# Kernel tuning notes

Hardware: AMD Instinct MI355X
Metric: run time of the kernel (lower is better)

## Reference

```python
import jax, jax.numpy as jnp
import numpy as np


def setup_inputs() -> dict:
    key = jax.random.key(0)
    ks = jax.random.split(key, 5)
    B, H, W, C, R = 4, 64, 64, 256, 32
    x = jax.random.normal(ks[0], (B, H, W, C), dtype=jnp.float32)
    # 1x1 conv kernels stored as [C_in, C_out] matrices (equivalent math)
    w_f = jax.random.normal(ks[1], (C, R), dtype=jnp.float32) * (1.0 / np.sqrt(C))
    w_g = jax.random.normal(ks[2], (C, R), dtype=jnp.float32) * (1.0 / np.sqrt(C))
    w_h = jax.random.normal(ks[3], (C, R), dtype=jnp.float32) * (1.0 / np.sqrt(C))
    w_v = jax.random.normal(ks[4], (R, C), dtype=jnp.float32) * (1.0 / np.sqrt(R))
    gamma = jnp.zeros((1,), dtype=jnp.float32)
    return {"x": x, "w_f": w_f, "w_g": w_g, "w_h": w_h, "w_v": w_v, "gamma": gamma}


def reference(x, w_f, w_g, w_h, w_v, gamma):
    B, H, W, C = x.shape
    N = H * W
    xt = x.reshape(B, N, C)                       # flatten spatial tokens
    f = jnp.einsum('bnc,cr->bnr', xt, w_f)        # 1x1 conv == token-wise matmul
    g = jnp.einsum('bnc,cr->bnr', xt, w_g)
    h = jnp.einsum('bnc,cr->bnr', xt, w_h)
    scores = jnp.einsum('bnr,bmr->bnm', f, g)     # [B, N, N]
    # NOTE: original softmaxes over axis=1 (the query/row axis), not axis=-1
    attn = jax.nn.softmax(scores, axis=1)
    y = jnp.einsum('bnm,bmr->bnr', attn, h)       # [B, N, R]
    y = jnp.einsum('bnr,rc->bnc', y, w_v)         # output 1x1 conv
    y = y.reshape(B, H, W, C)
    return gamma * y + x
```

## Files before the change

kernel.cpp:

```cpp
#include <hip/hip_runtime.h>


#define BB 4
#define NN 4096
#define CC 256
#define RR 32
#define CSEG 4
#define MP 40
#define LOG2E 1.44269504088896340736f

typedef short short8 __attribute__((ext_vector_type(8)));
typedef unsigned short ushort8 __attribute__((ext_vector_type(8)));
typedef float floatx4 __attribute__((ext_vector_type(4)));

#define MFMA16 __builtin_amdgcn_mfma_f32_16x16x32_bf16

static __device__ __forceinline__ unsigned short f2bf(float f) {
  union { float f; unsigned u; } v; v.f = f;
  const unsigned r = v.u + 0x7fffu + ((v.u >> 16) & 1u);
  return (unsigned short)(r >> 16);
}
static __device__ __forceinline__ unsigned bfpack(float lo, float hi) {
  return __builtin_amdgcn_perm(__float_as_uint(hi), __float_as_uint(lo), 0x07060302u);
}

__global__ __launch_bounds__(256) void k_fgh(
    const float* __restrict__ x, const float* __restrict__ wf,
    const float* __restrict__ wg, const float* __restrict__ wh,
    const float* __restrict__ wv,
    unsigned short* __restrict__ f16, unsigned short* __restrict__ g16,
    unsigned short* __restrict__ hT16, unsigned short* __restrict__ wvfrag) {
  __shared__ unsigned short wflds[24576];
  const int tid = threadIdx.x, lane = tid & 63, wave = tid >> 6;
  const int col = lane & 15, q = lane >> 4;
  if (blockIdx.x < 8) {
    const int base = blockIdx.x * 1024 + tid * 4;
#pragma unroll
    for (int e = 0; e < 4; ++e) {
      const int r = base + e;
      const int t = (r >> 9) & 15, l2 = (r >> 3) & 63, j = r & 7;
      wvfrag[r] = f2bf(wv[((l2 >> 4) * 8 + j) * CC + t * 16 + (l2 & 15)]);
    }
  }
  for (int s4 = tid; s4 < 6144; s4 += 256) {
    const int mat = s4 >> 11;
    const int s = (s4 & 2047) << 2;
    const int rr = s >> 5, c = s & 31;
    const float* w = (mat == 0) ? wf : ((mat == 1) ? wg : wh);
    const float4 v = *(const float4*)(w + s);
    const int kc = rr >> 5, q2 = (rr >> 3) & 3, j = rr & 7;
    const int base = (mat * 16 + kc * 2) * 512 + q2 * 128 + j;
    const float vv[4] = {v.x, v.y, v.z, v.w};
#pragma unroll
    for (int e = 0; e < 4; ++e) {
      const int ce = c + e;
      wflds[base + (ce >> 4) * 512 + (ce & 15) * 8] = f2bf(vv[e]);
    }
  }
  __syncthreads();
  const int t0 = blockIdx.x * 64 + wave * 16;
  short8 af[8];
  const float* xr = x + (long)(t0 + col) * CC + q * 8;
#pragma unroll
  for (int kc = 0; kc < 8; ++kc) {
    float tmp[8];
    *(float4*)(tmp) = *(const float4*)(xr + kc * 32);
    *(float4*)(tmp + 4) = *(const float4*)(xr + kc * 32 + 4);
    short8 o;
#pragma unroll
    for (int j = 0; j < 8; ++j) o[j] = (short)f2bf(tmp[j]);
    af[kc] = o;
  }
  const floatx4 zero = {0.f, 0.f, 0.f, 0.f};
  floatx4 acc[3][2];
#pragma unroll
  for (int m = 0; m < 3; ++m) { acc[m][0] = zero; acc[m][1] = zero; }
#pragma unroll
  for (int kc = 0; kc < 8; ++kc) {
#pragma unroll
    for (int mat = 0; mat < 3; ++mat) {
#pragma unroll
      for (int nt = 0; nt < 2; ++nt) {
        const short8 bf = *(const short8*)(wflds + (mat * 16 + kc * 2 + nt) * 512 + lane * 8);
        acc[mat][nt] = MFMA16(af[kc], bf, acc[mat][nt], 0, 0, 0);
      }
    }
  }
  const int b = t0 >> 12;
#pragma unroll
  for (int nt = 0; nt < 2; ++nt) {
#pragma unroll
    for (int r = 0; r < 4; ++r) {
      const int tok = t0 + q * 4 + r;
      const int n = nt * 16 + col;
      f16[(long)tok * RR + n] = f2bf(acc[0][nt][r] * LOG2E);
      g16[(long)tok * RR + n] = f2bf(acc[1][nt][r]);
      hT16[((long)b * RR + n) * NN + (tok & (NN - 1))] = f2bf(acc[2][nt][r]);
    }
  }
}

__global__ __launch_bounds__(256) void k_colsum(
    const unsigned short* __restrict__ f16, const unsigned short* __restrict__ g16,
    float* __restrict__ psum) {
  const int tid = threadIdx.x, lane = tid & 63, wave = tid >> 6;
  const int col = lane & 15, q = lane >> 4;
  const int mblk = blockIdx.x & 31;
  const int b = (blockIdx.x >> 5) & 3;
  const int seg = blockIdx.x >> 7;
  const int m0 = mblk * 128 + wave * 32;
  const short8 bg1 = *(const short8*)(g16 + ((long)(b * NN + m0 + col)) * RR + q * 8);
  const short8 bg2 = *(const short8*)(g16 + ((long)(b * NN + m0 + 16 + col)) * RR + q * 8);
  const floatx4 zero = {0.f, 0.f, 0.f, 0.f};
  float s1 = 0.f, s2 = 0.f;
  const unsigned short* fb = f16 + ((long)b * NN + seg * (NN / CSEG)) * RR;
#pragma unroll 4
  for (int n = 0; n < NN / CSEG; n += 16) {
    const short8 af = *(const short8*)(fb + (long)(n + col) * RR + q * 8);
    const floatx4 d1 = MFMA16(af, bg1, zero, 0, 0, 0);
    const floatx4 d2 = MFMA16(af, bg2, zero, 0, 0, 0);
    s1 += __builtin_amdgcn_exp2f(d1[0]) + __builtin_amdgcn_exp2f(d1[1]) +
          __builtin_amdgcn_exp2f(d1[2]) + __builtin_amdgcn_exp2f(d1[3]);
    s2 += __builtin_amdgcn_exp2f(d2[0]) + __builtin_amdgcn_exp2f(d2[1]) +
          __builtin_amdgcn_exp2f(d2[2]) + __builtin_amdgcn_exp2f(d2[3]);
  }
  s1 += __shfl_xor(s1, 16); s1 += __shfl_xor(s1, 32);
  s2 += __shfl_xor(s2, 16); s2 += __shfl_xor(s2, 32);
  if (lane < 16) {
    psum[(long)seg * (BB * NN) + b * NN + m0 + lane] = s1;
    psum[(long)seg * (BB * NN) + b * NN + m0 + 16 + lane] = s2;
  }
}

__global__ __launch_bounds__(256) void k_scaleh(
    const float* __restrict__ psum, unsigned short* __restrict__ hT16) {
  const long i8 = ((long)blockIdx.x * 256 + threadIdx.x) * 8;
  const int b = (int)(i8 >> 17);
  const int m = (int)(i8 & (NN - 1));
  float cs[8] = {0.f, 0.f, 0.f, 0.f, 0.f, 0.f, 0.f, 0.f};
#pragma unroll
  for (int sg = 0; sg < CSEG; ++sg) {
    const float* p = psum + (long)sg * (BB * NN) + b * NN + m;
    const float4 a = *(const float4*)p;
    const float4 c = *(const float4*)(p + 4);
    cs[0] += a.x; cs[1] += a.y; cs[2] += a.z; cs[3] += a.w;
    cs[4] += c.x; cs[5] += c.y; cs[6] += c.z; cs[7] += c.w;
  }
  const ushort8 hv = *(const ushort8*)(hT16 + i8);
  ushort8 o;
#pragma unroll
  for (int j = 0; j < 8; ++j) {
    const float h = __uint_as_float(((unsigned)hv[j]) << 16);
    o[j] = f2bf(h * __builtin_amdgcn_rcpf(cs[j]));
  }
  *(ushort8*)(hT16 + i8) = o;
}

struct PvU {
  union {
    unsigned short pt[4][32 * MP];
    float ot[4][16 * 132];
  };
};
#define C_ADDR(TN, TM) (((TN) + col) * MP + (TM) + q * 4)
__global__ __launch_bounds__(256, 2) void k_pvout(
    const unsigned short* __restrict__ f16, const unsigned short* __restrict__ g16,
    const unsigned short* __restrict__ hT16, const unsigned short* __restrict__ wvfrag,
    const float* __restrict__ x, const float* __restrict__ gamma,
    float* __restrict__ out) {
  __shared__ float ylds[4][32 * 36];
  __shared__ PvU u;
  const int tid = threadIdx.x, lane = tid & 63, wave = tid >> 6;
  const int col = lane & 15, q = lane >> 4;
  const int b = blockIdx.x >> 7;
  const int t0 = (blockIdx.x & 127) * 32;
  const floatx4 zero = {0.f, 0.f, 0.f, 0.f};
  const short8 af1 = *(const short8*)(f16 + ((long)(b * NN + t0 + col)) * RR + q * 8);
  const short8 af2 = *(const short8*)(f16 + ((long)(b * NN + t0 + 16 + col)) * RR + q * 8);
  floatx4 a11 = zero, a12 = zero, a21 = zero, a22 = zero;
  unsigned short* pt = &u.pt[wave][0];
  const unsigned short* gb = g16 + (long)b * NN * RR;
  const unsigned short* hb = hT16 + (long)b * RR * NN;
  const int mq = wave * 1024;
#pragma unroll 2
  for (int mi = 0; mi < 1024; mi += 32) {
    const int m0 = mq + mi;
    const short8 bg1 = *(const short8*)(gb + (long)(m0 + col) * RR + q * 8);
    const short8 bg2 = *(const short8*)(gb + (long)(m0 + 16 + col) * RR + q * 8);
    const floatx4 d00 = MFMA16(bg1, af1, zero, 0, 0, 0);
    const floatx4 d01 = MFMA16(bg2, af1, zero, 0, 0, 0);
    const floatx4 d10 = MFMA16(bg1, af2, zero, 0, 0, 0);
    const floatx4 d11 = MFMA16(bg2, af2, zero, 0, 0, 0);
    float w0, w1, w2, w3;
    w0 = __builtin_amdgcn_exp2f(d00[0]); w1 = __builtin_amdgcn_exp2f(d00[1]);
    w2 = __builtin_amdgcn_exp2f(d00[2]); w3 = __builtin_amdgcn_exp2f(d00[3]);
    *(uint2*)(pt + C_ADDR(0, 0)) = make_uint2(bfpack(w0, w1), bfpack(w2, w3));
    w0 = __builtin_amdgcn_exp2f(d01[0]); w1 = __builtin_amdgcn_exp2f(d01[1]);
    w2 = __builtin_amdgcn_exp2f(d01[2]); w3 = __builtin_amdgcn_exp2f(d01[3]);
    *(uint2*)(pt + C_ADDR(0, 16)) = make_uint2(bfpack(w0, w1), bfpack(w2, w3));
    w0 = __builtin_amdgcn_exp2f(d10[0]); w1 = __builtin_amdgcn_exp2f(d10[1]);
    w2 = __builtin_amdgcn_exp2f(d10[2]); w3 = __builtin_amdgcn_exp2f(d10[3]);
    *(uint2*)(pt + C_ADDR(16, 0)) = make_uint2(bfpack(w0, w1), bfpack(w2, w3));
    w0 = __builtin_amdgcn_exp2f(d11[0]); w1 = __builtin_amdgcn_exp2f(d11[1]);
    w2 = __builtin_amdgcn_exp2f(d11[2]); w3 = __builtin_amdgcn_exp2f(d11[3]);
    *(uint2*)(pt + C_ADDR(16, 16)) = make_uint2(bfpack(w0, w1), bfpack(w2, w3));
    const short8 ap1 = *(const short8*)(pt + col * MP + q * 8);
    const short8 ap2 = *(const short8*)(pt + (col + 16) * MP + q * 8);
    const short8 bh1 = *(const short8*)(hb + (long)col * NN + m0 + q * 8);
    const short8 bh2 = *(const short8*)(hb + (long)(col + 16) * NN + m0 + q * 8);
    a11 = MFMA16(ap1, bh1, a11, 0, 0, 0);
    a12 = MFMA16(ap1, bh2, a12, 0, 0, 0);
    a21 = MFMA16(ap2, bh1, a21, 0, 0, 0);
    a22 = MFMA16(ap2, bh2, a22, 0, 0, 0);
  }
  {
    float* yp = &ylds[wave][0];
#pragma unroll
    for (int r = 0; r < 4; ++r) {
      yp[(q * 4 + r) * 36 + col] = a11[r];
      yp[(q * 4 + r) * 36 + col + 16] = a12[r];
      yp[(16 + q * 4 + r) * 36 + col] = a21[r];
      yp[(16 + q * 4 + r) * 36 + col + 16] = a22[r];
    }
  }
  __syncthreads();
  {
    const int tile = wave & 1, hh = wave >> 1;
    float s[8] = {0.f, 0.f, 0.f, 0.f, 0.f, 0.f, 0.f, 0.f};
#pragma unroll
    for (int w2 = 0; w2 < 4; ++w2) {
      const float* yp = &ylds[w2][(tile * 16 + col) * 36 + q * 8];
      const float4 u0 = *(const float4*)yp;
      const float4 u1 = *(const float4*)(yp + 4);
      s[0] += u0.x; s[1] += u0.y; s[2] += u0.z; s[3] += u0.w;
      s[4] += u1.x; s[5] += u1.y; s[6] += u1.z; s[7] += u1.w;
    }
    short8 ay;
#pragma unroll
    for (int j = 0; j < 8; ++j) ay[j] = (short)f2bf(s[j]);
    const float gm = gamma[0];
    float* pw = &u.ot[wave][0];
#pragma unroll
    for (int t = 0; t < 8; ++t) {
      const short8 bw = *(const short8*)(wvfrag + (hh * 8 + t) * 512 + lane * 8);
      const floatx4 d = MFMA16(ay, bw, zero, 0, 0, 0);
#pragma unroll
      for (int r = 0; r < 4; ++r) pw[(q * 4 + r) * 132 + t * 16 + col] = d[r];
    }
    const int tok = lane >> 2, cg2 = (lane & 3) * 4;
#pragma unroll
    for (int j = 0; j < 8; ++j) {
      const float4 v = *(const float4*)(pw + tok * 132 + cg2 + j * 16);
      const long gidx = (long)(b * NN + t0 + tile * 16 + tok) * CC + hh * 128 + cg2 + j * 16;
      const float4 xv = *(const float4*)(x + gidx);
      float4 o;
      o.x = gm * v.x + xv.x; o.y = gm * v.y + xv.y;
      o.z = gm * v.z + xv.z; o.w = gm * v.w + xv.w;
      *(float4*)(out + gidx) = o;
    }
  }
}

extern "C" void kernel_launch(void* const* d_in, const int* in_sizes, int n_in,
                              void* d_out, int out_size, void* d_ws, size_t ws_size,
                              hipStream_t stream) {
  const float* x = (const float*)d_in[0];
  const float* wf = (const float*)d_in[1];
  const float* wg = (const float*)d_in[2];
  const float* wh = (const float*)d_in[3];
  const float* wv = (const float*)d_in[4];
  const float* gamma = (const float*)d_in[5];
  float* out = (float*)d_out;

  unsigned short* f16 = (unsigned short*)d_ws;
  unsigned short* g16 = f16 + (long)BB * NN * RR;
  unsigned short* hT16 = g16 + (long)BB * NN * RR;
  unsigned short* wvfrag = hT16 + (long)BB * NN * RR;
  float* psum = (float*)(wvfrag + 8192);

  k_fgh<<<BB * NN / 64, 256, 0, stream>>>(x, wf, wg, wh, wv, f16, g16, hT16, wvfrag);
  k_colsum<<<CSEG * BB * 32, 256, 0, stream>>>(f16, g16, psum);
  k_scaleh<<<BB * RR * NN / 2048, 256, 0, stream>>>(psum, hT16);
  k_pvout<<<BB * 128, 256, 0, stream>>>(f16, g16, hT16, wvfrag, x, gamma, out);
}
```

Baseline: 128.2 us.

## Precompute weight fragments in a prep kernel and shrink pvout LDS for occupancy

Adds a small k_prep kernel that converts wf/wg/wh and wv to bf16 MFMA-fragment layout once. This lets each k_fgh block copy a ready-made fragment buffer into LDS instead of repeating the scattered conversion in all 256 blocks. In k_pvout, the output-projection staging now reuses the per-wave P tile buffer in small 32-column chunks, which drops the larger union. The launch bound is raised to 4 blocks per CU to allow more occupancy. The cost is one extra kernel launch and possible register pressure under the tighter launch bound.

```diff
diff --git a/kernel.cpp b/kernel.cpp
--- a/kernel.cpp
+++ b/kernel.cpp
@@ -24,38 +24,39 @@
   return __builtin_amdgcn_perm(__float_as_uint(hi), __float_as_uint(lo), 0x07060302u);
 }
 
+__global__ __launch_bounds__(256) void k_prep(
+    const float* __restrict__ wf, const float* __restrict__ wg,
+    const float* __restrict__ wh, const float* __restrict__ wv,
+    unsigned short* __restrict__ wfrag, unsigned short* __restrict__ wvfrag) {
+  const int idx = blockIdx.x * 256 + threadIdx.x;
+  const int lane = (idx >> 3) & 63;
+  const int j = idx & 7;
+  const int col = lane & 15, q = lane >> 4;
+  if (idx < 24576) {
+    const int mat = idx >> 13;
+    const int fid = (idx >> 9) & 15;
+    const int kc = fid >> 1, nt = fid & 1;
+    const float* w = (mat == 0) ? wf : ((mat == 1) ? wg : wh);
+    wfrag[idx] = f2bf(w[(kc * 32 + q * 8 + j) * RR + nt * 16 + col]);
+  } else {
+    const int r = idx - 24576;
+    const int t = (r >> 9) & 15;
+    wvfrag[r] = f2bf(wv[(q * 8 + j) * CC + t * 16 + col]);
+  }
+}
+
 __global__ __launch_bounds__(256) void k_fgh(
-    const float* __restrict__ x, const float* __restrict__ wf,
-    const float* __restrict__ wg, const float* __restrict__ wh,
-    const float* __restrict__ wv,
+    const float* __restrict__ x, const unsigned short* __restrict__ wfrag,
     unsigned short* __restrict__ f16, unsigned short* __restrict__ g16,
-    unsigned short* __restrict__ hT16, unsigned short* __restrict__ wvfrag) {
+    unsigned short* __restrict__ hT16) {
   __shared__ unsigned short wflds[24576];
   const int tid = threadIdx.x, lane = tid & 63, wave = tid >> 6;
   const int col = lane & 15, q = lane >> 4;
-  if (blockIdx.x < 8) {
-    const int base = blockIdx.x * 1024 + tid * 4;
-#pragma unroll
-    for (int e = 0; e < 4; ++e) {
-      const int r = base + e;
-      const int t = (r >> 9) & 15, l2 = (r >> 3) & 63, j = r & 7;
-      wvfrag[r] = f2bf(wv[((l2 >> 4) * 8 + j) * CC + t * 16 + (l2 & 15)]);
-    }
-  }
-  for (int s4 = tid; s4 < 6144; s4 += 256) {
-    const int mat = s4 >> 11;
-    const int s = (s4 & 2047) << 2;
-    const int rr = s >> 5, c = s & 31;
-    const float* w = (mat == 0) ? wf : ((mat == 1) ? wg : wh);
-    const float4 v = *(const float4*)(w + s);
-    const int kc = rr >> 5, q2 = (rr >> 3) & 3, j = rr & 7;
-    const int base = (mat * 16 + kc * 2) * 512 + q2 * 128 + j;
-    const float vv[4] = {v.x, v.y, v.z, v.w};
-#pragma unroll
-    for (int e = 0; e < 4; ++e) {
-      const int ce = c + e;
-      wflds[base + (ce >> 4) * 512 + (ce & 15) * 8] = f2bf(vv[e]);
-    }
+  {
+    const uint4* src = (const uint4*)wfrag;
+    uint4* dst = (uint4*)wflds;
+#pragma unroll
+    for (int i = 0; i < 12; ++i) dst[tid + i * 256] = src[tid + i * 256];
   }
   __syncthreads();
   const int t0 = blockIdx.x * 64 + wave * 16;
@@ -156,20 +157,14 @@
   *(ushort8*)(hT16 + i8) = o;
 }
 
-struct PvU {
-  union {
-    unsigned short pt[4][32 * MP];
-    float ot[4][16 * 132];
-  };
-};
 #define C_ADDR(TN, TM) (((TN) + col) * MP + (TM) + q * 4)
-__global__ __launch_bounds__(256, 2) void k_pvout(
+__global__ __launch_bounds__(256, 4) void k_pvout(
     const unsigned short* __restrict__ f16, const unsigned short* __restrict__ g16,
     const unsigned short* __restrict__ hT16, const unsigned short* __restrict__ wvfrag,
     const float* __restrict__ x, const float* __restrict__ gamma,
     float* __restrict__ out) {
   __shared__ float ylds[4][32 * 36];
-  __shared__ PvU u;
+  __shared__ unsigned short pt_all[4][32 * MP];
   const int tid = threadIdx.x, lane = tid & 63, wave = tid >> 6;
   const int col = lane & 15, q = lane >> 4;
   const int b = blockIdx.x >> 7;
@@ -178,7 +173,7 @@
   const short8 af1 = *(const short8*)(f16 + ((long)(b * NN + t0 + col)) * RR + q * 8);
   const short8 af2 = *(const short8*)(f16 + ((long)(b * NN + t0 + 16 + col)) * RR + q * 8);
   floatx4 a11 = zero, a12 = zero, a21 = zero, a22 = zero;
-  unsigned short* pt = &u.pt[wave][0];
+  unsigned short* pt = &pt_all[wave][0];
   const unsigned short* gb = g16 + (long)b * NN * RR;
   const unsigned short* hb = hT16 + (long)b * RR * NN;
   const int mq = wave * 1024;
@@ -239,24 +234,30 @@
 #pragma unroll
     for (int j = 0; j < 8; ++j) ay[j] = (short)f2bf(s[j]);
     const float gm = gamma[0];
-    float* pw = &u.ot[wave][0];
-#pragma unroll
-    for (int t = 0; t < 8; ++t) {
-      const short8 bw = *(const short8*)(wvfrag + (hh * 8 + t) * 512 + lane * 8);
-      const floatx4 d = MFMA16(ay, bw, zero, 0, 0, 0);
-#pragma unroll
-      for (int r = 0; r < 4; ++r) pw[(q * 4 + r) * 132 + t * 16 + col] = d[r];
-    }
-    const int tok = lane >> 2, cg2 = (lane & 3) * 4;
-#pragma unroll
-    for (int j = 0; j < 8; ++j) {
-      const float4 v = *(const float4*)(pw + tok * 132 + cg2 + j * 16);
-      const long gidx = (long)(b * NN + t0 + tile * 16 + tok) * CC + hh * 128 + cg2 + j * 16;
-      const float4 xv = *(const float4*)(x + gidx);
-      float4 o;
-      o.x = gm * v.x + xv.x; o.y = gm * v.y + xv.y;
-      o.z = gm * v.z + xv.z; o.w = gm * v.w + xv.w;
-      *(float4*)(out + gidx) = o;
+    float* sc = (float*)pt;
+    const int row = lane >> 2, c4 = (lane & 3) * 4;
+#pragma unroll
+    for (int tp = 0; tp < 8; tp += 2) {
+      const short8 bw0 = *(const short8*)(wvfrag + (hh * 8 + tp) * 512 + lane * 8);
+      const short8 bw1 = *(const short8*)(wvfrag + (hh * 8 + tp + 1) * 512 + lane * 8);
+      const floatx4 d0 = MFMA16(ay, bw0, zero, 0, 0, 0);
+      const floatx4 d1 = MFMA16(ay, bw1, zero, 0, 0, 0);
+#pragma unroll
+      for (int r = 0; r < 4; ++r) {
+        sc[(q * 4 + r) * 36 + col] = d0[r];
+        sc[(q * 4 + r) * 36 + col + 16] = d1[r];
+      }
+#pragma unroll
+      for (int j = 0; j < 2; ++j) {
+        const float4 v = *(const float4*)(sc + row * 36 + c4 + j * 16);
+        const long gidx = (long)(b * NN + t0 + tile * 16 + row) * CC +
+                          hh * 128 + tp * 16 + j * 16 + c4;
+        const float4 xv = *(const float4*)(x + gidx);
+        float4 o;
+        o.x = gm * v.x + xv.x; o.y = gm * v.y + xv.y;
+        o.z = gm * v.z + xv.z; o.w = gm * v.w + xv.w;
+        *(float4*)(out + gidx) = o;
+      }
     }
   }
 }
@@ -275,10 +276,12 @@
   unsigned short* f16 = (unsigned short*)d_ws;
   unsigned short* g16 = f16 + (long)BB * NN * RR;
   unsigned short* hT16 = g16 + (long)BB * NN * RR;
-  unsigned short* wvfrag = hT16 + (long)BB * NN * RR;
+  unsigned short* wfrag = hT16 + (long)BB * NN * RR;
+  unsigned short* wvfrag = wfrag + 24576;
   float* psum = (float*)(wvfrag + 8192);
 
-  k_fgh<<<BB * NN / 64, 256, 0, stream>>>(x, wf, wg, wh, wv, f16, g16, hT16, wvfrag);
+  k_prep<<<128, 256, 0, stream>>>(wf, wg, wh, wv, wfrag, wvfrag);
+  k_fgh<<<BB * NN / 64, 256, 0, stream>>>(x, wfrag, f16, g16, hT16);
   k_colsum<<<CSEG * BB * 32, 256, 0, stream>>>(f16, g16, psum);
   k_scaleh<<<BB * RR * NN / 2048, 256, 0, stream>>>(psum, hT16);
   k_pvout<<<BB * 128, 256, 0, stream>>>(f16, g16, hT16, wvfrag, x, gamma, out);
```

Result: faster. 124.3 us (-3.1%).
